# Performance work log

Measured on AMD Instinct MI355X. Metric: run time of the kernel, lower is better.

## Reference

```python
import jax, jax.numpy as jnp
import numpy as np

# Llama-3-8B-like attention, prefill over B sequences of length S (flattened tokens)
D = 4096      # hidden_size
N = 32        # num query heads
K = 8         # num KV heads (GQA)
H = 128       # head_dim (== head_dim_original, already a multiple of 128 so no padding)
B = 4         # sequences in the ragged batch
S = 1024      # tokens per sequence
T = B * S     # total flattened tokens
ROPE_THETA = 10000.0


def _apply_rope(x, positions, head_dim, theta):
    # x: [T, n_heads, H]; positions: [T] int
    inv_freq = 1.0 / (theta ** (jnp.arange(0, head_dim, 2, dtype=jnp.float32) / head_dim))
    freqs = positions.astype(jnp.float32)[:, None] * inv_freq[None, :]  # [T, H/2]
    emb = jnp.concatenate([freqs, freqs], axis=-1)                       # [T, H]
    cos = jnp.cos(emb)[:, None, :].astype(x.dtype)
    sin = jnp.sin(emb)[:, None, :].astype(x.dtype)
    x1, x2 = jnp.split(x, 2, axis=-1)
    rotated = jnp.concatenate([-x2, x1], axis=-1)
    return x * cos + rotated * sin


def setup_inputs() -> dict:
    key = jax.random.key(0)
    ks = jax.random.split(key, 5)
    x = jax.random.normal(ks[0], (T, D), dtype=jnp.float32)
    # positions restart per sequence (ragged prefill metadata)
    input_positions = (jnp.arange(T, dtype=jnp.int32) % S)
    w_scale = 0.02
    Wq = jax.random.normal(ks[1], (D, N, H), dtype=jnp.float32) * w_scale
    Wk = jax.random.normal(ks[2], (D, K, H), dtype=jnp.float32) * w_scale
    Wv = jax.random.normal(ks[3], (D, K, H), dtype=jnp.float32) * w_scale
    Wo = jax.random.normal(ks[4], (N, H, D), dtype=jnp.float32) * w_scale
    return {"x": x, "input_positions": input_positions,
            "Wq": Wq, "Wk": Wk, "Wv": Wv, "Wo": Wo}


def reference(x, input_positions, Wq, Wk, Wv, Wo):
    # QKV projections (flattened tokens)
    q = jnp.einsum('td,dnh->tnh', x, Wq)   # [T, N, H]
    k = jnp.einsum('td,dkh->tkh', x, Wk)   # [T, K, H]
    v = jnp.einsum('td,dkh->tkh', x, Wv)   # [T, K, H]
    q = _apply_rope(q, input_positions, H, ROPE_THETA)
    k = _apply_rope(k, input_positions, H, ROPE_THETA)

    # Ragged causal attention: per-sequence causal SDPA with GQA head grouping.
    G = N // K  # query heads per KV head
    qb = q.reshape(B, S, K, G, H)
    kb = k.reshape(B, S, K, H)
    vb = v.reshape(B, S, K, H)
    scale = jnp.asarray(H, q.dtype) ** -0.5  # head_dim_original ** -0.5
    scores = jnp.einsum('bqkgh,bskh->bkgqs', qb, kb) * scale  # [B,K,G,S,S]
    causal = jnp.tril(jnp.ones((S, S), dtype=bool))
    scores = jnp.where(causal, scores, jnp.finfo(scores.dtype).min)
    probs = jax.nn.softmax(scores, axis=-1)
    out = jnp.einsum('bkgqs,bskh->bqkgh', probs, vb).reshape(T, N, H)

    # Output projection
    o = jnp.einsum('tnh,nhd->td', out, Wo)  # [T, D]
    return o
```

## Files before the change

kernel.cpp:

```cpp
#include <hip/hip_runtime.h>
#include <cstdint>


typedef unsigned short u16;
typedef short bf16x8 __attribute__((ext_vector_type(8)));
typedef float f32x4 __attribute__((ext_vector_type(4)));

#define L2E 1.44269504088896340736f

static __device__ __forceinline__ u16 f2bf(float f) {
  union { float f; unsigned u; } v; v.f = f;
  unsigned r = (v.u + 0x7fffu + ((v.u >> 16) & 1u)) >> 16;
  return (u16)r;
}
static __device__ __forceinline__ float bf2f(u16 h) {
  union { unsigned u; float f; } v; v.u = ((unsigned)h) << 16;
  return v.f;
}

typedef __attribute__((address_space(1))) const unsigned int gas_u32;
typedef __attribute__((address_space(3))) unsigned int las_u32;
static __device__ __forceinline__ void glds16(const void* g, const void* l) {
  __builtin_amdgcn_global_load_lds((gas_u32*)(uintptr_t)g,
                                   (las_u32*)(unsigned)(uintptr_t)l, 16, 0, 0);
}

__global__ __launch_bounds__(256) void cvt_kernel(const float4* __restrict__ in,
                                                  uint2* __restrict__ out, int n4) {
  int i = blockIdx.x * 256 + threadIdx.x;
  if (i < n4) {
    float4 v = in[i];
    uint2 r;
    r.x = (unsigned)f2bf(v.x) | ((unsigned)f2bf(v.y) << 16);
    r.y = (unsigned)f2bf(v.z) | ((unsigned)f2bf(v.w) << 16);
    out[i] = r;
  }
}

__global__ __launch_bounds__(256) void tcvt_kernel(const float* __restrict__ in,
                                                   u16* __restrict__ out, int R, int C) {
  __shared__ float tile[64][68];
  int tx = threadIdx.x & 15, ty = threadIdx.x >> 4;
  int r0 = blockIdx.y * 64, c0 = blockIdx.x * 64;
#pragma unroll
  for (int k = 0; k < 4; ++k) {
    float4 v = *(const float4*)&in[(size_t)(r0 + ty + k * 16) * C + c0 + tx * 4];
    *(float4*)&tile[ty + k * 16][tx * 4] = v;
  }
  __syncthreads();
#pragma unroll
  for (int k = 0; k < 4; ++k) {
    int ocol = ty + k * 16;
    ushort4 o;
    o.x = f2bf(tile[tx * 4 + 0][ocol]);
    o.y = f2bf(tile[tx * 4 + 1][ocol]);
    o.z = f2bf(tile[tx * 4 + 2][ocol]);
    o.w = f2bf(tile[tx * 4 + 3][ocol]);
    *(ushort4*)&out[(size_t)(c0 + ocol) * R + r0 + tx * 4] = o;
  }
}

__global__ __launch_bounds__(256) void ropetab_kernel(float2* __restrict__ tab) {
  int idx = blockIdx.x * 256 + threadIdx.x;
  int i = idx & 63;
  float inv = exp2f(-0.20751874963942190927f * (float)i);
  float f = (float)(idx >> 6) * inv;
  float s, c;
  sincosf(f, &s, &c);
  tab[idx] = make_float2(c, s);
}

template <int BF16OUT, int ROPE>
__global__ __launch_bounds__(512, 2) void gemm_nt8(const u16* __restrict__ A,
                                                   const u16* __restrict__ Bm,
                                                   void* __restrict__ Cp,
                                                   int M, int N, int Kd,
                                                   const int* __restrict__ posi,
                                                   const float2* __restrict__ rtab) {
  __shared__ u16 Als[2][2][8192];
  __shared__ u16 Bls[2][2][8192];
  const int tid = threadIdx.x;
  const int w = tid >> 6, lane = tid & 63;
  const int ln15 = lane & 15, quad = lane >> 4;
  const int wm = w & 1, wn = w >> 1;

  const int nbm = M >> 8;
  const int nwg = nbm * (N >> 8);
  const int cpx = nwg >> 3;
  const int bid = blockIdx.x;
  const int swz = (bid & 7) * cpx + (bid >> 3);
  const int bm = swz & (nbm - 1);
  const int bn = swz / nbm;
  const int m0 = bm << 8, n0 = bn << 8;

  const int nt = Kd >> 6;

  const int srow = lane >> 2;
  const int schk = ((lane & 3) ^ ((lane >> 3) & 3)) << 3;
  const u16* aSrc = A + (size_t)(m0 + w * 32 + srow) * Kd + schk;
  const u16* bSrc = Bm + (size_t)(n0 + w * 32 + srow) * Kd + schk;
  const int ldsb = w * 1024;

  const int rswz = (quad ^ ((ln15 >> 1) & 3)) << 3;
  const int aoff = (wm * 128 + ln15) * 32 + rswz;
  const int boff = ((wn >> 1) * 128 + (wn & 1) * 32 + ln15) * 32 + rswz;
  const unsigned aAddr = (unsigned)(uintptr_t)&Als[0][0][aoff];
  const unsigned bAddr = (unsigned)(uintptr_t)&Bls[0][0][boff];

  f32x4 acc[8][4];
#pragma unroll
  for (int i = 0; i < 8; ++i)
#pragma unroll
    for (int j = 0; j < 4; ++j) acc[i][j] = f32x4{0.f, 0.f, 0.f, 0.f};
  bf16x8 af[8];

#define DSR(dst, addr, off) \
  asm volatile("ds_read_b128 %0, %1 offset:%2" : "=v"(dst) : "v"(addr), "i"(off))

#define STA(kt, buf, ks)                                          \
  do {                                                            \
    int kc_ = (kt) < nt ? (kt) : nt - 1;                          \
    const u16* s_ = aSrc + (size_t)kc_ * 64 + (ks) * 32;          \
    glds16(s_, &Als[buf][ks][ldsb]);                              \
    glds16(s_ + (size_t)16 * Kd, &Als[buf][ks][ldsb + 512]);      \
  } while (0)
#define STB(kt, buf, ks)                                          \
  do {                                                            \
    int kc_ = (kt) < nt ? (kt) : nt - 1;                          \
    const u16* s_ = bSrc + (size_t)kc_ * 64 + (ks) * 32;          \
    glds16(s_, &Bls[buf][ks][ldsb]);                              \
    glds16(s_ + (size_t)16 * Kd, &Bls[buf][ks][ldsb + 512]);      \
  } while (0)

#define PHASE(buf, ks, nh, STAGE, VM)                                              \
  do {                                                                             \
    if ((nh) == 0) {                                                               \
      DSR(af[0], aAddr, (buf)*32768 + (ks)*16384 + 0 * 1024);                      \
      DSR(af[1], aAddr, (buf)*32768 + (ks)*16384 + 1 * 1024);                      \
      DSR(af[2], aAddr, (buf)*32768 + (ks)*16384 + 2 * 1024);                      \
      DSR(af[3], aAddr, (buf)*32768 + (ks)*16384 + 3 * 1024);                      \
      DSR(af[4], aAddr, (buf)*32768 + (ks)*16384 + 4 * 1024);                      \
      DSR(af[5], aAddr, (buf)*32768 + (ks)*16384 + 5 * 1024);                      \
      DSR(af[6], aAddr, (buf)*32768 + (ks)*16384 + 6 * 1024);                      \
      DSR(af[7], aAddr, (buf)*32768 + (ks)*16384 + 7 * 1024);                      \
    }                                                                              \
    bf16x8 b0_, b1_;                                                               \
    DSR(b0_, bAddr, (buf)*32768 + (ks)*16384 + (nh)*4096);                         \
    DSR(b1_, bAddr, (buf)*32768 + (ks)*16384 + (nh)*4096 + 1024);                  \
    STAGE;                                                                         \
    __builtin_amdgcn_s_barrier();                                                  \
    asm volatile("s_waitcnt lgkmcnt(0)" ::: "memory");                             \
    __builtin_amdgcn_sched_barrier(0);                                             \
    __builtin_amdgcn_s_setprio(1);                                                 \
    _Pragma("unroll") for (int m_ = 0; m_ < 8; ++m_) {                             \
      acc[m_][2 * (nh)] =                                                          \
          __builtin_amdgcn_mfma_f32_16x16x32_bf16(af[m_], b0_, acc[m_][2 * (nh)],  \
                                                  0, 0, 0);                        \
      acc[m_][2 * (nh) + 1] = __builtin_amdgcn_mfma_f32_16x16x32_bf16(             \
          af[m_], b1_, acc[m_][2 * (nh) + 1], 0, 0, 0);                            \
    }                                                                              \
    __builtin_amdgcn_s_setprio(0);                                                 \
    if (VM) asm volatile("s_waitcnt vmcnt(6)" ::: "memory");                       \
    __builtin_amdgcn_s_barrier();                                                  \
    __builtin_amdgcn_sched_barrier(0);                                             \
  } while (0)

  STA(0, 0, 0); STB(0, 0, 0); STA(0, 0, 1); STB(0, 0, 1);
  STA(1, 1, 0); STB(1, 1, 0); STA(1, 1, 1);
  asm volatile("s_waitcnt vmcnt(6)" ::: "memory");
  __builtin_amdgcn_s_barrier();
  __builtin_amdgcn_sched_barrier(0);

  const int iters = nt >> 1;
  for (int i = 0; i < iters; ++i) {
    const int t = 2 * i;
    PHASE(0, 0, 0, STB(t + 1, 1, 1), 0);
    PHASE(0, 0, 1, STA(t + 2, 0, 0), 0);
    PHASE(0, 1, 0, STB(t + 2, 0, 0), 0);
    PHASE(0, 1, 1, STA(t + 2, 0, 1), 1);
    PHASE(1, 0, 0, STB(t + 2, 0, 1), 0);
    PHASE(1, 0, 1, STA(t + 3, 1, 0), 0);
    PHASE(1, 1, 0, STB(t + 3, 1, 0), 0);
    PHASE(1, 1, 1, STA(t + 3, 1, 1), 1);
  }
#undef PHASE
#undef STA
#undef STB
#undef DSR

  const int crow = m0 + wm * 128 + quad * 4;
  const int ccol = n0 + (wn >> 1) * 128 + (wn & 1) * 32 + ln15;
  const int cat = (n0 < 4096) ? 0 : (n0 < 5120 ? 1 : 2);

  if (ROPE && cat < 2) {
    const float qs = (cat == 0) ? 0.08838834764831845f : 1.0f;
    const int i0 = (wn & 1) * 32 + ln15;
#pragma unroll
    for (int m = 0; m < 8; ++m)
#pragma unroll
      for (int r = 0; r < 4; ++r) {
        int row = crow + m * 16 + r;
        int p = posi[row];
#pragma unroll
        for (int s = 0; s < 2; ++s) {
          float2 cs = rtab[(p << 6) + i0 + s * 16];
          float x1 = acc[m][s][r], x2 = acc[m][s + 2][r];
          float o1 = (x1 * cs.x - x2 * cs.y) * qs;
          float o2 = (x2 * cs.x + x1 * cs.y) * qs;
          ((u16*)Cp)[(size_t)row * N + ccol + s * 16] = f2bf(o1);
          ((u16*)Cp)[(size_t)row * N + ccol + s * 16 + 64] = f2bf(o2);
        }
      }
  } else {
#pragma unroll
    for (int m = 0; m < 8; ++m)
#pragma unroll
      for (int j = 0; j < 4; ++j) {
        int col = ccol + (j & 1) * 16 + (j >> 1) * 64;
#pragma unroll
        for (int r = 0; r < 4; ++r) {
          float v = acc[m][j][r];
          if (BF16OUT)
            ((u16*)Cp)[(size_t)(crow + m * 16 + r) * N + col] = f2bf(v);
          else
            ((float*)Cp)[(size_t)(crow + m * 16 + r) * N + col] = v;
        }
      }
  }
}

__global__ __launch_bounds__(512, 2) void attn_kernel(const u16* __restrict__ qkv,
                                                      u16* __restrict__ outp) {
  __shared__ u16 Klds[2][64 * 128];
  __shared__ u16 Vtlds[128 * 72];
  __shared__ u16 Plds[8 * 32 * 72];

  const int bx = blockIdx.x;
  const int qb = 15 - (bx >> 5);
  const int kh = bx & 7;
  const int b = (bx >> 3) & 3;

  const int tid = threadIdx.x;
  const int w = tid >> 6;
  const int lane = tid & 63;
  const int ln15 = lane & 15;
  const int quad = lane >> 4;
  const int g = w & 3;
  const int half = w >> 2;
  const int n = kh * 4 + g;

  const int ldq = 6144;
  const int seq0 = b << 10;
  const int q0 = seq0 + qb * 64;

  const u16* Qg = qkv + n * 128;
  const u16* Kg = qkv + 4096 + kh * 128;
  const u16* Vg = qkv + 5120 + kh * 128;

  bf16x8 qf[2][4];
#pragma unroll
  for (int rf = 0; rf < 2; ++rf) {
    const u16* qrow = Qg + (size_t)(q0 + half * 32 + rf * 16 + ln15) * ldq + quad * 8;
#pragma unroll
    for (int ks = 0; ks < 4; ++ks) qf[rf][ks] = *(const bf16x8*)(qrow + ks * 32);
  }

  f32x4 o[2][8];
#pragma unroll
  for (int rf = 0; rf < 2; ++rf)
#pragma unroll
    for (int i = 0; i < 8; ++i) o[rf][i] = f32x4{0.f, 0.f, 0.f, 0.f};
  float m_r[2][4], l_r[2][4];
#pragma unroll
  for (int rf = 0; rf < 2; ++rf)
#pragma unroll
    for (int r = 0; r < 4; ++r) { m_r[rf][r] = -INFINITY; l_r[rf][r] = 0.f; }

  const int kr0 = w * 8 + (lane >> 4);
  const int kr1 = kr0 + 4;
  const u16* kp0 = Kg + (size_t)(seq0 + kr0) * ldq + (((lane & 15) ^ (kr0 & 7)) << 3);
  const u16* kp1 = Kg + (size_t)(seq0 + kr1) * ldq + (((lane & 15) ^ (kr1 & 7)) << 3);

  const int vs0 = (tid & 31) * 2;
  const int vhb = (tid >> 5) * 8;

  union V8 { uint4 v; u16 s[8]; };
  V8 ra, rb;
  {
    const u16* v0 = Vg + (size_t)(seq0 + vs0) * ldq + vhb;
    ra.v = *(const uint4*)v0;
    rb.v = *(const uint4*)(v0 + ldq);
    glds16(kp0, &Klds[0][(w * 8) * 128]);
    glds16(kp1, &Klds[0][(w * 8 + 4) * 128]);
  }

  for (int kt = 0; kt <= qb; ++kt) {
    const int cur = kt & 1;
    __syncthreads();
    {
#pragma unroll
      for (int j = 0; j < 8; ++j) {
        unsigned pk = (unsigned)ra.s[j] | ((unsigned)rb.s[j] << 16);
        *(unsigned*)&Vtlds[(vhb + j) * 72 + vs0] = pk;
      }
    }
    __syncthreads();

    if (kt < qb) {
      glds16(kp0 + (size_t)(kt + 1) * 64 * ldq, &Klds[cur ^ 1][(w * 8) * 128]);
      glds16(kp1 + (size_t)(kt + 1) * 64 * ldq, &Klds[cur ^ 1][(w * 8 + 4) * 128]);
      const u16* v0 = Vg + (size_t)(seq0 + (kt + 1) * 64 + vs0) * ldq + vhb;
      ra.v = *(const uint4*)v0;
      rb.v = *(const uint4*)(v0 + ldq);
    }

    f32x4 sfr[2][4];
#pragma unroll
    for (int rf = 0; rf < 2; ++rf)
#pragma unroll
      for (int c = 0; c < 4; ++c) {
        f32x4 acc = f32x4{0.f, 0.f, 0.f, 0.f};
#pragma unroll
        for (int ks = 0; ks < 4; ++ks) {
          int rr = c * 16 + ln15;
          int ph = (ks * 4 + quad) ^ (rr & 7);
          bf16x8 kf = *(const bf16x8*)&Klds[cur][rr * 128 + ph * 8];
          acc = __builtin_amdgcn_mfma_f32_16x16x32_bf16(qf[rf][ks], kf, acc, 0, 0, 0);
        }
        sfr[rf][c] = acc;
      }

    if (kt == qb) {
#pragma unroll
      for (int rf = 0; rf < 2; ++rf)
#pragma unroll
        for (int c = 0; c < 4; ++c) {
          int col = c * 16 + ln15;
#pragma unroll
          for (int r = 0; r < 4; ++r)
            if (col > half * 32 + rf * 16 + quad * 4 + r) sfr[rf][c][r] = -INFINITY;
        }
    }

    float mx[2][4];
#pragma unroll
    for (int rf = 0; rf < 2; ++rf)
#pragma unroll
      for (int r = 0; r < 4; ++r) {
        float m0 = fmaxf(fmaxf(sfr[rf][0][r], sfr[rf][1][r]),
                         fmaxf(sfr[rf][2][r], sfr[rf][3][r]));
        m0 = fmaxf(m0, __shfl_xor(m0, 1));
        m0 = fmaxf(m0, __shfl_xor(m0, 2));
        m0 = fmaxf(m0, __shfl_xor(m0, 4));
        m0 = fmaxf(m0, __shfl_xor(m0, 8));
        mx[rf][r] = m0;
      }
    float ex = -INFINITY;
#pragma unroll
    for (int rf = 0; rf < 2; ++rf)
#pragma unroll
      for (int r = 0; r < 4; ++r) ex = fmaxf(ex, mx[rf][r] - m_r[rf][r]);
    if (!__all(ex <= 8.f)) {
#pragma unroll
      for (int rf = 0; rf < 2; ++rf)
#pragma unroll
        for (int r = 0; r < 4; ++r) {
          float mnew = fmaxf(m_r[rf][r], mx[rf][r]);
          float al = exp2f((m_r[rf][r] - mnew) * L2E);
          m_r[rf][r] = mnew;
          l_r[rf][r] *= al;
#pragma unroll
          for (int ht = 0; ht < 8; ++ht) o[rf][ht][r] *= al;
        }
    }
#pragma unroll
    for (int rf = 0; rf < 2; ++rf)
#pragma unroll
      for (int r = 0; r < 4; ++r) {
        float rs = 0.f;
#pragma unroll
        for (int c = 0; c < 4; ++c) {
          float pv = exp2f((sfr[rf][c][r] - m_r[rf][r]) * L2E);
          sfr[rf][c][r] = pv;
          rs += pv;
        }
        rs += __shfl_xor(rs, 1);
        rs += __shfl_xor(rs, 2);
        rs += __shfl_xor(rs, 4);
        rs += __shfl_xor(rs, 8);
        l_r[rf][r] += rs;
      }

#pragma unroll
    for (int rf = 0; rf < 2; ++rf)
#pragma unroll
      for (int c = 0; c < 4; ++c)
#pragma unroll
        for (int r = 0; r < 4; ++r)
          Plds[w * 2304 + (rf * 16 + quad * 4 + r) * 72 + c * 16 + ln15] =
              f2bf(sfr[rf][c][r]);

    asm volatile("s_waitcnt lgkmcnt(0)" ::: "memory");

    bf16x8 pf[2][2];
#pragma unroll
    for (int rf = 0; rf < 2; ++rf)
#pragma unroll
      for (int ks = 0; ks < 2; ++ks)
        pf[rf][ks] =
            *(const bf16x8*)&Plds[w * 2304 + (rf * 16 + ln15) * 72 + ks * 32 + quad * 8];
#pragma unroll
    for (int ht = 0; ht < 8; ++ht)
#pragma unroll
      for (int ks = 0; ks < 2; ++ks) {
        bf16x8 vf = *(const bf16x8*)&Vtlds[(ht * 16 + ln15) * 72 + ks * 32 + quad * 8];
#pragma unroll
        for (int rf = 0; rf < 2; ++rf)
          o[rf][ht] = __builtin_amdgcn_mfma_f32_16x16x32_bf16(pf[rf][ks], vf, o[rf][ht],
                                                              0, 0, 0);
      }
  }

#pragma unroll
  for (int rf = 0; rf < 2; ++rf)
#pragma unroll
    for (int r = 0; r < 4; ++r) l_r[rf][r] = 1.f / l_r[rf][r];
#pragma unroll
  for (int rf = 0; rf < 2; ++rf)
#pragma unroll
    for (int ht = 0; ht < 8; ++ht)
#pragma unroll
      for (int r = 0; r < 4; ++r)
        outp[(size_t)(q0 + half * 32 + rf * 16 + quad * 4 + r) * 4096 + n * 128 +
             ht * 16 + ln15] = f2bf(o[rf][ht][r] * l_r[rf][r]);
}

extern "C" void kernel_launch(void* const* d_in, const int* in_sizes, int n_in,
                              void* d_out, int out_size, void* d_ws, size_t ws_size,
                              hipStream_t stream) {
  const float* x = (const float*)d_in[0];
  const int* posi = (const int*)d_in[1];
  const float* Wq = (const float*)d_in[2];
  const float* Wk = (const float*)d_in[3];
  const float* Wv = (const float*)d_in[4];
  const float* Wo = (const float*)d_in[5];
  float* out = (float*)d_out;
  char* ws = (char*)d_ws;

  u16* xb = (u16*)(ws);
  u16* Wt = (u16*)(ws + 33554432);
  u16* WoT = (u16*)(ws + 83886080);
  u16* qkv = (u16*)(ws + 117440512);
  u16* attn = xb;
  float2* rtab = (float2*)d_out;

  cvt_kernel<<<16384, 256, 0, stream>>>((const float4*)x, (uint2*)xb, 4194304);
  tcvt_kernel<<<dim3(64, 64), 256, 0, stream>>>(Wq, Wt, 4096, 4096);
  tcvt_kernel<<<dim3(16, 64), 256, 0, stream>>>(Wk, Wt + (size_t)4096 * 4096, 4096, 1024);
  tcvt_kernel<<<dim3(16, 64), 256, 0, stream>>>(Wv, Wt + (size_t)5120 * 4096, 4096, 1024);
  tcvt_kernel<<<dim3(64, 64), 256, 0, stream>>>(Wo, WoT, 4096, 4096);
  ropetab_kernel<<<256, 256, 0, stream>>>(rtab);

  gemm_nt8<1, 1><<<dim3(384), 512, 0, stream>>>(xb, Wt, qkv, 4096, 6144, 4096, posi, rtab);
  attn_kernel<<<512, 512, 0, stream>>>(qkv, attn);
  gemm_nt8<0, 0><<<dim3(256), 512, 0, stream>>>(attn, WoT, out, 4096, 4096, 4096,
                                                nullptr, nullptr);
}
```

Before: 665.9 us.

## Software-pipeline PV MFMA with next QK, double-buffer V, merge prep kernels

The attention loop now double-buffers the transposed V tile, which removes one barrier per iteration. The P·V MFMAs of the previous tile are deferred so they run after the current tile's QK MFMAs under raised wave priority, with a final PV step after the loop. The per-row sum shuffle reduction moves out of the loop into the epilogue. The four weight transpose-convert launches and the RoPE table launch are merged into one prep kernel to cut launch overhead, at the cost of extra LDS and registers, since pf is now live across iterations.

```diff
diff --git a/kernel.cpp b/kernel.cpp
--- a/kernel.cpp
+++ b/kernel.cpp
@@ -37,11 +37,36 @@
   }
 }
 
-__global__ __launch_bounds__(256) void tcvt_kernel(const float* __restrict__ in,
-                                                   u16* __restrict__ out, int R, int C) {
+__global__ __launch_bounds__(256) void prep_kernel(const float* __restrict__ Wq,
+                                                   const float* __restrict__ Wk,
+                                                   const float* __restrict__ Wv,
+                                                   const float* __restrict__ Wo,
+                                                   u16* __restrict__ Wt,
+                                                   u16* __restrict__ WoT,
+                                                   float2* __restrict__ rtab) {
+  const int bx = blockIdx.x;
+  if (bx >= 10240) {
+    int idx = (bx - 10240) * 256 + threadIdx.x;
+    int i = idx & 63;
+    float inv = exp2f(-0.20751874963942190927f * (float)i);
+    float f = (float)(idx >> 6) * inv;
+    float s, c;
+    sincosf(f, &s, &c);
+    rtab[idx] = make_float2(c, s);
+    return;
+  }
+  const float* in;
+  u16* out;
+  int C, t;
+  if (bx < 4096)      { in = Wq; out = Wt;                        C = 4096; t = bx; }
+  else if (bx < 5120) { in = Wk; out = Wt + (size_t)4096 * 4096;  C = 1024; t = bx - 4096; }
+  else if (bx < 6144) { in = Wv; out = Wt + (size_t)5120 * 4096;  C = 1024; t = bx - 5120; }
+  else                { in = Wo; out = WoT;                       C = 4096; t = bx - 6144; }
+  const int ctiles = C >> 6;
+  const int c0 = (t % ctiles) * 64, r0 = (t / ctiles) * 64;
+
   __shared__ float tile[64][68];
   int tx = threadIdx.x & 15, ty = threadIdx.x >> 4;
-  int r0 = blockIdx.y * 64, c0 = blockIdx.x * 64;
 #pragma unroll
   for (int k = 0; k < 4; ++k) {
     float4 v = *(const float4*)&in[(size_t)(r0 + ty + k * 16) * C + c0 + tx * 4];
@@ -56,18 +81,8 @@
     o.y = f2bf(tile[tx * 4 + 1][ocol]);
     o.z = f2bf(tile[tx * 4 + 2][ocol]);
     o.w = f2bf(tile[tx * 4 + 3][ocol]);
-    *(ushort4*)&out[(size_t)(c0 + ocol) * R + r0 + tx * 4] = o;
-  }
-}
-
-__global__ __launch_bounds__(256) void ropetab_kernel(float2* __restrict__ tab) {
-  int idx = blockIdx.x * 256 + threadIdx.x;
-  int i = idx & 63;
-  float inv = exp2f(-0.20751874963942190927f * (float)i);
-  float f = (float)(idx >> 6) * inv;
-  float s, c;
-  sincosf(f, &s, &c);
-  tab[idx] = make_float2(c, s);
+    *(ushort4*)&out[(size_t)(c0 + ocol) * 4096 + r0 + tx * 4] = o;
+  }
 }
 
 template <int BF16OUT, int ROPE>
@@ -232,7 +247,7 @@
 __global__ __launch_bounds__(512, 2) void attn_kernel(const u16* __restrict__ qkv,
                                                       u16* __restrict__ outp) {
   __shared__ u16 Klds[2][64 * 128];
-  __shared__ u16 Vtlds[128 * 72];
+  __shared__ u16 Vtlds[2][128 * 72];
   __shared__ u16 Plds[8 * 32 * 72];
 
   const int bx = blockIdx.x;
@@ -294,26 +309,30 @@
     glds16(kp1, &Klds[0][(w * 8 + 4) * 128]);
   }
 
+  bf16x8 pf[2][2];
+
   for (int kt = 0; kt <= qb; ++kt) {
     const int cur = kt & 1;
     __syncthreads();
-    {
-#pragma unroll
-      for (int j = 0; j < 8; ++j) {
-        unsigned pk = (unsigned)ra.s[j] | ((unsigned)rb.s[j] << 16);
-        *(unsigned*)&Vtlds[(vhb + j) * 72 + vs0] = pk;
-      }
-    }
-    __syncthreads();
 
     if (kt < qb) {
       glds16(kp0 + (size_t)(kt + 1) * 64 * ldq, &Klds[cur ^ 1][(w * 8) * 128]);
       glds16(kp1 + (size_t)(kt + 1) * 64 * ldq, &Klds[cur ^ 1][(w * 8 + 4) * 128]);
+    }
+    {
+#pragma unroll
+      for (int j = 0; j < 8; ++j) {
+        unsigned pk = (unsigned)ra.s[j] | ((unsigned)rb.s[j] << 16);
+        *(unsigned*)&Vtlds[cur][(vhb + j) * 72 + vs0] = pk;
+      }
+    }
+    if (kt < qb) {
       const u16* v0 = Vg + (size_t)(seq0 + (kt + 1) * 64 + vs0) * ldq + vhb;
       ra.v = *(const uint4*)v0;
       rb.v = *(const uint4*)(v0 + ldq);
     }
 
+    __builtin_amdgcn_s_setprio(1);
     f32x4 sfr[2][4];
 #pragma unroll
     for (int rf = 0; rf < 2; ++rf)
@@ -329,6 +348,20 @@
         }
         sfr[rf][c] = acc;
       }
+    if (kt > 0) {
+#pragma unroll
+      for (int ht = 0; ht < 8; ++ht)
+#pragma unroll
+        for (int ks = 0; ks < 2; ++ks) {
+          bf16x8 vf =
+              *(const bf16x8*)&Vtlds[cur ^ 1][(ht * 16 + ln15) * 72 + ks * 32 + quad * 8];
+#pragma unroll
+          for (int rf = 0; rf < 2; ++rf)
+            o[rf][ht] =
+                __builtin_amdgcn_mfma_f32_16x16x32_bf16(pf[rf][ks], vf, o[rf][ht], 0, 0, 0);
+        }
+    }
+    __builtin_amdgcn_s_setprio(0);
 
     if (kt == qb) {
 #pragma unroll
@@ -384,10 +417,6 @@
           sfr[rf][c][r] = pv;
           rs += pv;
         }
-        rs += __shfl_xor(rs, 1);
-        rs += __shfl_xor(rs, 2);
-        rs += __shfl_xor(rs, 4);
-        rs += __shfl_xor(rs, 8);
         l_r[rf][r] += rs;
       }
 
@@ -402,29 +431,41 @@
 
     asm volatile("s_waitcnt lgkmcnt(0)" ::: "memory");
 
-    bf16x8 pf[2][2];
 #pragma unroll
     for (int rf = 0; rf < 2; ++rf)
 #pragma unroll
       for (int ks = 0; ks < 2; ++ks)
         pf[rf][ks] =
             *(const bf16x8*)&Plds[w * 2304 + (rf * 16 + ln15) * 72 + ks * 32 + quad * 8];
+  }
+
+  __syncthreads();
+  {
+    const int cur = qb & 1;
 #pragma unroll
     for (int ht = 0; ht < 8; ++ht)
 #pragma unroll
       for (int ks = 0; ks < 2; ++ks) {
-        bf16x8 vf = *(const bf16x8*)&Vtlds[(ht * 16 + ln15) * 72 + ks * 32 + quad * 8];
+        bf16x8 vf =
+            *(const bf16x8*)&Vtlds[cur][(ht * 16 + ln15) * 72 + ks * 32 + quad * 8];
 #pragma unroll
         for (int rf = 0; rf < 2; ++rf)
-          o[rf][ht] = __builtin_amdgcn_mfma_f32_16x16x32_bf16(pf[rf][ks], vf, o[rf][ht],
-                                                              0, 0, 0);
+          o[rf][ht] =
+              __builtin_amdgcn_mfma_f32_16x16x32_bf16(pf[rf][ks], vf, o[rf][ht], 0, 0, 0);
       }
   }
 
 #pragma unroll
   for (int rf = 0; rf < 2; ++rf)
 #pragma unroll
-    for (int r = 0; r < 4; ++r) l_r[rf][r] = 1.f / l_r[rf][r];
+    for (int r = 0; r < 4; ++r) {
+      float s = l_r[rf][r];
+      s += __shfl_xor(s, 1);
+      s += __shfl_xor(s, 2);
+      s += __shfl_xor(s, 4);
+      s += __shfl_xor(s, 8);
+      l_r[rf][r] = 1.f / s;
+    }
 #pragma unroll
   for (int rf = 0; rf < 2; ++rf)
 #pragma unroll
@@ -455,11 +496,7 @@
   float2* rtab = (float2*)d_out;
 
   cvt_kernel<<<16384, 256, 0, stream>>>((const float4*)x, (uint2*)xb, 4194304);
-  tcvt_kernel<<<dim3(64, 64), 256, 0, stream>>>(Wq, Wt, 4096, 4096);
-  tcvt_kernel<<<dim3(16, 64), 256, 0, stream>>>(Wk, Wt + (size_t)4096 * 4096, 4096, 1024);
-  tcvt_kernel<<<dim3(16, 64), 256, 0, stream>>>(Wv, Wt + (size_t)5120 * 4096, 4096, 1024);
-  tcvt_kernel<<<dim3(64, 64), 256, 0, stream>>>(Wo, WoT, 4096, 4096);
-  ropetab_kernel<<<256, 256, 0, stream>>>(rtab);
+  prep_kernel<<<10496, 256, 0, stream>>>(Wq, Wk, Wv, Wo, Wt, WoT, rtab);
 
   gemm_nt8<1, 1><<<dim3(384), 512, 0, stream>>>(xb, Wt, qkv, 4096, 6144, 4096, posi, rtab);
   attn_kernel<<<512, 512, 0, stream>>>(qkv, attn);
```

Result: faster. 644.8 us (-3.2%).
